# Kernel optimization log

Measured on AMD Instinct MI355X. Metric: run time of the kernel, lower is better.

The kernel has to match this reference:

```python
import jax, jax.numpy as jnp
import numpy as np

N = 4096          # n_assets
D_MODEL = 512
DK = 128
EMB_DIM = 32
QC = 4.0          # quantization_coeff
NUM_EMB = int(np.floor((N - 1) / QC)) + 1  # 1024


def setup_inputs() -> dict:
    key = jax.random.key(0)
    ks = jax.random.split(key, 9)

    def lin_w(k, out_d, in_d):
        # torch nn.Linear default init ~ U(-1/sqrt(in_d), 1/sqrt(in_d))
        b = 1.0 / np.sqrt(in_d)
        return jax.random.uniform(k, (out_d, in_d), jnp.float32, -b, b)

    return {
        "stock_reprs": jax.random.normal(ks[0], (N, D_MODEL), jnp.float32),
        "price_rising_ranks": jax.random.uniform(ks[1], (N,), jnp.float32, 0.0, float(N)),
        "Wq_w": lin_w(ks[2], DK, D_MODEL), "Wq_b": jnp.zeros((DK,), jnp.float32),
        "Wk_w": lin_w(ks[3], DK, D_MODEL), "Wk_b": jnp.zeros((DK,), jnp.float32),
        "Wv_w": lin_w(ks[4], D_MODEL, D_MODEL), "Wv_b": jnp.zeros((D_MODEL,), jnp.float32),
        "rank_emb": jax.random.normal(ks[5], (NUM_EMB, EMB_DIM), jnp.float32),
        "wL_w": lin_w(ks[6], 1, EMB_DIM), "wL_b": jnp.zeros((1,), jnp.float32),
        "wf_w": lin_w(ks[7], 1, D_MODEL), "wf_b": jnp.zeros((1,), jnp.float32),
    }


def reference(stock_reprs, price_rising_ranks, Wq_w, Wq_b, Wk_w, Wk_b,
              Wv_w, Wv_b, rank_emb, wL_w, wL_b, wf_w, wf_b):
    # QKV projections: [N, dk], [N, dk], [N, d_model]
    q = stock_reprs @ Wq_w.T + Wq_b
    k = stock_reprs @ Wk_w.T + Wk_b
    v = stock_reprs @ Wv_w.T + Wv_b

    # Quantized pairwise rank-distance indices [N, N]
    diff = jnp.abs(price_rising_ranks[:, None] - price_rising_ranks[None, :])
    d_ij = jnp.clip(jnp.floor(diff / QC).astype(jnp.int32), 0, NUM_EMB - 1)

    # Gate per quantized distance: sigmoid(w_L(Emb[d])). Precompute the
    # [NUM_EMB] table instead of materializing the [N, N, EMB_DIM] gather
    # (same math: the lookup-then-linear commutes with the gather).
    gate_table = jax.nn.sigmoid(rank_emb @ wL_w[0] + wL_b[0])  # [NUM_EMB]
    psi = gate_table[d_ij]                                     # [N, N]

    score = (q @ k.T) / np.sqrt(float(DK))                     # [N, N]
    att = jax.nn.softmax(psi * score, axis=-1)                 # [N, N]
    a = att @ v                                                # [N, d_model]
    return jax.nn.sigmoid(a @ wf_w[0] + wf_b[0])               # [N]
```

## Files before the change

kernel.cpp:

```cpp
#include <hip/hip_runtime.h>

#define N_ASSETS 4096
#define DMODEL 512
#define DKQ 128
#define NUM_EMB 1024

typedef float f32x4 __attribute__((ext_vector_type(4)));
typedef short s16x8 __attribute__((ext_vector_type(8)));

__device__ __forceinline__ unsigned short f2bf(float x) {
    unsigned u = __float_as_uint(x);
    u += 0x7FFF + ((u >> 16) & 1);
    return (unsigned short)(u >> 16);
}

__device__ __forceinline__ s16x8 ld8(const unsigned short* p) {
    return *(const s16x8*)p;
}

__global__ __launch_bounds__(256) void k_prep(const float* __restrict__ remb,
                                              const float* __restrict__ wLw,
                                              const float* __restrict__ wLb,
                                              const float* __restrict__ Wq,
                                              const float* __restrict__ Wk,
                                              const float* __restrict__ bq,
                                              const float* __restrict__ bk,
                                              const float* __restrict__ Wv,
                                              const float* __restrict__ bv,
                                              const float* __restrict__ wfw,
                                              float* __restrict__ gate,
                                              unsigned short* __restrict__ Wb,
                                              float* __restrict__ bias,
                                              float* __restrict__ weff) {
    int bid = blockIdx.x;
    int tid = threadIdx.x;
    if (bid < 4) {
        int e = bid * 256 + tid;
        float s = wLb[0];
#pragma unroll
        for (int j = 0; j < 32; ++j) s += remb[e * 32 + j] * wLw[j];
        gate[e] = 1.f / (1.f + __expf(-s));
    } else if (bid < 132) {
        int gid = (bid - 4) * 256 + tid;
        int i4 = gid * 4;
        int row = i4 >> 9;
        int col = i4 & 511;
        const float* src; int r;
        if (row < 128) { src = Wq; r = row; } else { src = Wk; r = row - 128; }
        float4 v = *(const float4*)(src + r * 512 + col);
        ushort4 o;
        o.x = f2bf(v.x); o.y = f2bf(v.y); o.z = f2bf(v.z); o.w = f2bf(v.w);
        *(ushort4*)(Wb + i4) = o;
        if (gid < 256) bias[gid] = (gid < 128) ? bq[gid] : bk[gid - 128];
    } else if (bid < 134) {
        __shared__ float wf_s[512];
        wf_s[tid] = wfw[tid];
        wf_s[tid + 256] = wfw[tid + 256];
        __syncthreads();
        int din = (bid - 132) * 256 + tid;
        float a0 = 0.f, a1 = 0.f, a2 = 0.f, a3 = 0.f;
        for (int dout = 0; dout < 512; dout += 4) {
            a0 += Wv[(dout + 0) * 512 + din] * wf_s[dout + 0];
            a1 += Wv[(dout + 1) * 512 + din] * wf_s[dout + 1];
            a2 += Wv[(dout + 2) * 512 + din] * wf_s[dout + 2];
            a3 += Wv[(dout + 3) * 512 + din] * wf_s[dout + 3];
        }
        weff[din] = (a0 + a1) + (a2 + a3);
    } else {
        if (tid < 64) {
            float s = 0.f;
#pragma unroll
            for (int j = 0; j < 8; ++j) s += bv[tid * 8 + j] * wfw[tid * 8 + j];
#pragma unroll
            for (int m = 1; m < 64; m <<= 1) s += __shfl_xor(s, m);
            if (tid == 0) weff[512] = s;
        }
    }
}

__global__ void k_convx(const float* __restrict__ X, unsigned short* __restrict__ Xb, int n) {
    int i4 = (blockIdx.x * 256 + threadIdx.x) * 4;
    if (i4 < n) {
        float4 v = *(const float4*)(X + i4);
        ushort4 o;
        o.x = f2bf(v.x); o.y = f2bf(v.y); o.z = f2bf(v.z); o.w = f2bf(v.w);
        *(ushort4*)(Xb + i4) = o;
    }
}

__global__ __launch_bounds__(256) void k_qk(const unsigned short* __restrict__ Xb,
                                            const unsigned short* __restrict__ Wb,
                                            const float* __restrict__ bias,
                                            unsigned short* __restrict__ qb,
                                            unsigned short* __restrict__ kb) {
    int tid = threadIdx.x;
    int lane = tid & 63, w = tid >> 6;
    int l15 = lane & 15, lhi = lane >> 4;
    int m0 = blockIdx.x * 64 + w * 16;
    int n0 = blockIdx.y * 64;

    f32x4 zero4 = {0.f, 0.f, 0.f, 0.f};
    f32x4 acc[4];
#pragma unroll
    for (int s = 0; s < 4; ++s) acc[s] = zero4;

    const unsigned short* arow = Xb + (m0 + l15) * 512 + lhi * 8;
    for (int k0 = 0; k0 < 512; k0 += 32) {
        s16x8 af = ld8(arow + k0);
#pragma unroll
        for (int s = 0; s < 4; ++s) {
            s16x8 bf = ld8(Wb + (n0 + 16 * s + l15) * 512 + k0 + lhi * 8);
            acc[s] = __builtin_amdgcn_mfma_f32_16x16x32_bf16(af, bf, acc[s], 0, 0, 0);
        }
    }
#pragma unroll
    for (int s = 0; s < 4; ++s) {
        int n = n0 + 16 * s + l15;
        float bv_ = bias[n];
#pragma unroll
        for (int r = 0; r < 4; ++r) {
            int m = m0 + lhi * 4 + r;
            unsigned short val = f2bf(acc[s][r] + bv_);
            if (n < 128) qb[m * 128 + n] = val;
            else         kb[m * 128 + (n - 128)] = val;
        }
    }
}

__global__ __launch_bounds__(256) void k_ugemv(const float* __restrict__ X,
                                               const float* __restrict__ weff,
                                               float* __restrict__ u) {
    int lane = threadIdx.x & 63, w = threadIdx.x >> 6;
    int row = blockIdx.x * 4 + w;
    const float4* ap = (const float4*)(X + row * 512 + lane * 8);
    const float4* wp = (const float4*)(weff + lane * 8);
    float4 a0 = ap[0], a1 = ap[1], w0 = wp[0], w1 = wp[1];
    float s = a0.x * w0.x + a0.y * w0.y + a0.z * w0.z + a0.w * w0.w
            + a1.x * w1.x + a1.y * w1.y + a1.z * w1.z + a1.w * w1.w;
#pragma unroll
    for (int m = 1; m < 64; m <<= 1) s += __shfl_xor(s, m);
    if (lane == 0) u[row] = s + weff[512];
}

__global__ __launch_bounds__(256) void k_score(const unsigned short* __restrict__ qb,
                                               const unsigned short* __restrict__ kb,
                                               const float* __restrict__ ranks,
                                               const float* __restrict__ gate,
                                               const float* __restrict__ u,
                                               float* __restrict__ num_part,
                                               float* __restrict__ den_part) {
    __shared__ float g_lds[NUM_EMB];
    __shared__ float rr[128], rc[128], uc[128];
    int tid = threadIdx.x;
    int lane = tid & 63, w = tid >> 6;
    int l15 = lane & 15, lhi = lane >> 4;
    int wm = w >> 1, wn = w & 1;
    int bm = blockIdx.x, bn = blockIdx.y;

    for (int i = tid; i < NUM_EMB; i += 256) g_lds[i] = gate[i];
    if (tid < 128) {
        rr[tid] = ranks[bm * 128 + tid];
        rc[tid] = ranks[bn * 128 + tid];
        uc[tid] = u[bn * 128 + tid];
    }
    __syncthreads();

    int row0 = wm * 64;
    int col0 = wn * 64;

    f32x4 zero4 = {0.f, 0.f, 0.f, 0.f};
    f32x4 acc[4][4];
#pragma unroll
    for (int mi = 0; mi < 4; ++mi)
#pragma unroll
        for (int ni = 0; ni < 4; ++ni) acc[mi][ni] = zero4;

#pragma unroll
    for (int k0 = 0; k0 < DKQ; k0 += 32) {
        s16x8 af[4], bf[4];
#pragma unroll
        for (int mi = 0; mi < 4; ++mi)
            af[mi] = ld8(qb + (bm * 128 + row0 + mi * 16 + l15) * DKQ + k0 + lhi * 8);
#pragma unroll
        for (int ni = 0; ni < 4; ++ni)
            bf[ni] = ld8(kb + (bn * 128 + col0 + ni * 16 + l15) * DKQ + k0 + lhi * 8);
#pragma unroll
        for (int mi = 0; mi < 4; ++mi)
#pragma unroll
            for (int ni = 0; ni < 4; ++ni)
                acc[mi][ni] = __builtin_amdgcn_mfma_f32_16x16x32_bf16(af[mi], bf[ni], acc[mi][ni], 0, 0, 0);
    }

    const float scale = 0.08838834764831845f;
    float num[4][4], den[4][4];
#pragma unroll
    for (int mi = 0; mi < 4; ++mi)
#pragma unroll
        for (int r = 0; r < 4; ++r) { num[mi][r] = 0.f; den[mi][r] = 0.f; }

#pragma unroll
    for (int mi = 0; mi < 4; ++mi) {
#pragma unroll
        for (int ni = 0; ni < 4; ++ni) {
            int coll = col0 + ni * 16 + l15;
            float rj = rc[coll];
            float uj = uc[coll];
#pragma unroll
            for (int r = 0; r < 4; ++r) {
                int rowl = row0 + mi * 16 + lhi * 4 + r;
                float s = acc[mi][ni][r] * scale;
                float diff = fabsf(rr[rowl] - rj);
                int d = min((int)(diff * 0.25f), NUM_EMB - 1);
                float p = __expf(g_lds[d] * s);
                den[mi][r] += p;
                num[mi][r] += p * uj;
            }
        }
    }
#pragma unroll
    for (int mi = 0; mi < 4; ++mi) {
#pragma unroll
        for (int r = 0; r < 4; ++r) {
            float vn = num[mi][r], vd = den[mi][r];
            vn += __shfl_xor(vn, 1); vd += __shfl_xor(vd, 1);
            vn += __shfl_xor(vn, 2); vd += __shfl_xor(vd, 2);
            vn += __shfl_xor(vn, 4); vd += __shfl_xor(vd, 4);
            vn += __shfl_xor(vn, 8); vd += __shfl_xor(vd, 8);
            if (l15 == 0) {
                int row = bm * 128 + row0 + mi * 16 + lhi * 4 + r;
                num_part[(bn * 2 + wn) * N_ASSETS + row] = vn;
                den_part[(bn * 2 + wn) * N_ASSETS + row] = vd;
            }
        }
    }
}

__global__ __launch_bounds__(256) void k_out(const float* __restrict__ num_part,
                                             const float* __restrict__ den_part,
                                             const float* __restrict__ wfb,
                                             float* __restrict__ out) {
    int lane = threadIdx.x & 63, w = threadIdx.x >> 6;
    int row = blockIdx.x * 4 + w;
    float vn = num_part[lane * N_ASSETS + row];
    float vd = den_part[lane * N_ASSETS + row];
#pragma unroll
    for (int m = 1; m < 64; m <<= 1) {
        vn += __shfl_xor(vn, m);
        vd += __shfl_xor(vd, m);
    }
    if (lane == 0) out[row] = 1.f / (1.f + __expf(-(vn / vd + wfb[0])));
}

extern "C" void kernel_launch(void* const* d_in, const int* in_sizes, int n_in,
                              void* d_out, int out_size, void* d_ws, size_t ws_size,
                              hipStream_t stream) {
    const float* X    = (const float*)d_in[0];
    const float* rks  = (const float*)d_in[1];
    const float* Wq_w = (const float*)d_in[2];
    const float* Wq_b = (const float*)d_in[3];
    const float* Wk_w = (const float*)d_in[4];
    const float* Wk_b = (const float*)d_in[5];
    const float* Wv_w = (const float*)d_in[6];
    const float* Wv_b = (const float*)d_in[7];
    const float* remb = (const float*)d_in[8];
    const float* wL_w = (const float*)d_in[9];
    const float* wL_b = (const float*)d_in[10];
    const float* wf_w = (const float*)d_in[11];
    const float* wf_b = (const float*)d_in[12];
    float* out = (float*)d_out;
    char* ws = (char*)d_ws;

    const size_t OFF_GATE = 0;
    const size_t OFF_BIAS = 4096;
    const size_t OFF_WEFF = 8192;
    const size_t OFF_XB   = 12288;
    const size_t OFF_WB   = OFF_XB + 4194304;
    const size_t OFF_QB   = OFF_WB + 262144;
    const size_t OFF_KB   = OFF_QB + 1048576;
    const size_t OFF_U    = OFF_KB + 1048576;
    const size_t OFF_NUM  = OFF_U + 16384;
    const size_t OFF_DEN  = OFF_NUM + 1048576;

    float* gate = (float*)(ws + OFF_GATE);
    float* bias = (float*)(ws + OFF_BIAS);
    float* weff = (float*)(ws + OFF_WEFF);
    unsigned short* Xb = (unsigned short*)(ws + OFF_XB);
    unsigned short* Wb = (unsigned short*)(ws + OFF_WB);
    unsigned short* qb = (unsigned short*)(ws + OFF_QB);
    unsigned short* kb = (unsigned short*)(ws + OFF_KB);
    float* u = (float*)(ws + OFF_U);
    float* num_part = (float*)(ws + OFF_NUM);
    float* den_part = (float*)(ws + OFF_DEN);

    k_prep<<<135, 256, 0, stream>>>(remb, wL_w, wL_b, Wq_w, Wk_w, Wq_b, Wk_b,
                                    Wv_w, Wv_b, wf_w, gate, Wb, bias, weff);
    k_convx<<<2048, 256, 0, stream>>>(X, Xb, N_ASSETS * DMODEL);
    k_qk<<<dim3(64, 4), 256, 0, stream>>>(Xb, Wb, bias, qb, kb);
    k_ugemv<<<1024, 256, 0, stream>>>(X, weff, u);
    k_score<<<dim3(32, 32), 256, 0, stream>>>(qb, kb, rks, gate, u, num_part, den_part);
    k_out<<<1024, 256, 0, stream>>>(num_part, den_part, wf_b, out);
}
```

Before: 71.71 us.

## Fuse X conversion, QK projection and u GEMV into one projection kernel

```diff
diff --git a/kernel.cpp b/kernel.cpp
--- a/kernel.cpp
+++ b/kernel.cpp
@@ -1,10 +1,13 @@
 #include <hip/hip_runtime.h>
+#include <hip/hip_bf16.h>
 
 #define N_ASSETS 4096
 #define DMODEL 512
 #define DKQ 128
 #define NUM_EMB 1024
 
+#define SCLQ 0.12752789f
+
 typedef float f32x4 __attribute__((ext_vector_type(4)));
 typedef short s16x8 __attribute__((ext_vector_type(8)));
 
@@ -12,6 +15,11 @@
     unsigned u = __float_as_uint(x);
     u += 0x7FFF + ((u >> 16) & 1);
     return (unsigned short)(u >> 16);
+}
+
+__device__ __forceinline__ unsigned pk2(float lo, float hi) {
+    __hip_bfloat162 h = __float22bfloat162_rn(make_float2(lo, hi));
+    return *(unsigned*)&h;
 }
 
 __device__ __forceinline__ s16x8 ld8(const unsigned short* p) {
@@ -52,20 +60,29 @@
         o.x = f2bf(v.x); o.y = f2bf(v.y); o.z = f2bf(v.z); o.w = f2bf(v.w);
         *(ushort4*)(Wb + i4) = o;
         if (gid < 256) bias[gid] = (gid < 128) ? bq[gid] : bk[gid - 128];
-    } else if (bid < 134) {
+    } else if (bid < 148) {
         __shared__ float wf_s[512];
+        __shared__ float part[8][32];
         wf_s[tid] = wfw[tid];
         wf_s[tid + 256] = wfw[tid + 256];
         __syncthreads();
-        int din = (bid - 132) * 256 + tid;
-        float a0 = 0.f, a1 = 0.f, a2 = 0.f, a3 = 0.f;
-        for (int dout = 0; dout < 512; dout += 4) {
-            a0 += Wv[(dout + 0) * 512 + din] * wf_s[dout + 0];
-            a1 += Wv[(dout + 1) * 512 + din] * wf_s[dout + 1];
-            a2 += Wv[(dout + 2) * 512 + din] * wf_s[dout + 2];
-            a3 += Wv[(dout + 3) * 512 + din] * wf_s[dout + 3];
-        }
-        weff[din] = (a0 + a1) + (a2 + a3);
+        int din = (bid - 132) * 32 + (tid & 31);
+        int slice = tid >> 5;
+        const float* wp = Wv + din;
+        float a = 0.f;
+#pragma unroll 4
+        for (int j = 0; j < 64; ++j) {
+            int dout = slice * 64 + j;
+            a += wp[(size_t)dout * 512] * wf_s[dout];
+        }
+        part[slice][tid & 31] = a;
+        __syncthreads();
+        if (tid < 32) {
+            float s = 0.f;
+#pragma unroll
+            for (int sl = 0; sl < 8; ++sl) s += part[sl][tid];
+            weff[(bid - 132) * 32 + tid] = s;
+        }
     } else {
         if (tid < 64) {
             float s = 0.f;
@@ -78,68 +95,74 @@
     }
 }
 
-__global__ void k_convx(const float* __restrict__ X, unsigned short* __restrict__ Xb, int n) {
-    int i4 = (blockIdx.x * 256 + threadIdx.x) * 4;
-    if (i4 < n) {
-        float4 v = *(const float4*)(X + i4);
-        ushort4 o;
-        o.x = f2bf(v.x); o.y = f2bf(v.y); o.z = f2bf(v.z); o.w = f2bf(v.w);
-        *(ushort4*)(Xb + i4) = o;
-    }
-}
-
-__global__ __launch_bounds__(256) void k_qk(const unsigned short* __restrict__ Xb,
-                                            const unsigned short* __restrict__ Wb,
-                                            const float* __restrict__ bias,
-                                            unsigned short* __restrict__ qb,
-                                            unsigned short* __restrict__ kb) {
+__global__ __launch_bounds__(256) void k_proj(const float* __restrict__ X,
+                                              const float* __restrict__ weff,
+                                              const unsigned short* __restrict__ Wb,
+                                              const float* __restrict__ bias,
+                                              unsigned short* __restrict__ qb,
+                                              unsigned short* __restrict__ kb,
+                                              float* __restrict__ u) {
     int tid = threadIdx.x;
     int lane = tid & 63, w = tid >> 6;
     int l15 = lane & 15, lhi = lane >> 4;
-    int m0 = blockIdx.x * 64 + w * 16;
-    int n0 = blockIdx.y * 64;
-
+    int m0 = blockIdx.x * 16;
+
+    const float* xrow = X + (size_t)(m0 + l15) * DMODEL + lhi * 8;
+    const float* wrow = weff + lhi * 8;
+
+    s16x8 af[16];
+    float us = 0.f;
+    bool dou = (w == 0);
+#pragma unroll
+    for (int kc = 0; kc < 16; ++kc) {
+        float4 a = *(const float4*)(xrow + kc * 32);
+        float4 b = *(const float4*)(xrow + kc * 32 + 4);
+        if (dou) {
+            float4 wa = *(const float4*)(wrow + kc * 32);
+            float4 wb = *(const float4*)(wrow + kc * 32 + 4);
+            us += a.x * wa.x + a.y * wa.y + a.z * wa.z + a.w * wa.w
+                + b.x * wb.x + b.y * wb.y + b.z * wb.z + b.w * wb.w;
+        }
+        union { s16x8 v; unsigned q[4]; } fr;
+        fr.q[0] = pk2(a.x, a.y);
+        fr.q[1] = pk2(a.z, a.w);
+        fr.q[2] = pk2(b.x, b.y);
+        fr.q[3] = pk2(b.z, b.w);
+        af[kc] = fr.v;
+    }
+    if (dou) {
+        us += __shfl_xor(us, 16);
+        us += __shfl_xor(us, 32);
+        if (lane < 16) u[m0 + lane] = us + weff[512];
+    }
+
+    int n0w = w * 64;
     f32x4 zero4 = {0.f, 0.f, 0.f, 0.f};
     f32x4 acc[4];
 #pragma unroll
-    for (int s = 0; s < 4; ++s) acc[s] = zero4;
-
-    const unsigned short* arow = Xb + (m0 + l15) * 512 + lhi * 8;
-    for (int k0 = 0; k0 < 512; k0 += 32) {
-        s16x8 af = ld8(arow + k0);
-#pragma unroll
-        for (int s = 0; s < 4; ++s) {
-            s16x8 bf = ld8(Wb + (n0 + 16 * s + l15) * 512 + k0 + lhi * 8);
-            acc[s] = __builtin_amdgcn_mfma_f32_16x16x32_bf16(af, bf, acc[s], 0, 0, 0);
-        }
-    }
-#pragma unroll
-    for (int s = 0; s < 4; ++s) {
-        int n = n0 + 16 * s + l15;
+    for (int ni = 0; ni < 4; ++ni) acc[ni] = zero4;
+
+#pragma unroll
+    for (int k0 = 0; k0 < 16; ++k0) {
+#pragma unroll
+        for (int ni = 0; ni < 4; ++ni) {
+            s16x8 bf = ld8(Wb + (size_t)(n0w + ni * 16 + l15) * 512 + k0 * 32 + lhi * 8);
+            acc[ni] = __builtin_amdgcn_mfma_f32_16x16x32_bf16(af[k0], bf, acc[ni], 0, 0, 0);
+        }
+    }
+
+#pragma unroll
+    for (int ni = 0; ni < 4; ++ni) {
+        int n = n0w + ni * 16 + l15;
         float bv_ = bias[n];
 #pragma unroll
         for (int r = 0; r < 4; ++r) {
             int m = m0 + lhi * 4 + r;
-            unsigned short val = f2bf(acc[s][r] + bv_);
-            if (n < 128) qb[m * 128 + n] = val;
-            else         kb[m * 128 + (n - 128)] = val;
-        }
-    }
-}
-
-__global__ __launch_bounds__(256) void k_ugemv(const float* __restrict__ X,
-                                               const float* __restrict__ weff,
-                                               float* __restrict__ u) {
-    int lane = threadIdx.x & 63, w = threadIdx.x >> 6;
-    int row = blockIdx.x * 4 + w;
-    const float4* ap = (const float4*)(X + row * 512 + lane * 8);
-    const float4* wp = (const float4*)(weff + lane * 8);
-    float4 a0 = ap[0], a1 = ap[1], w0 = wp[0], w1 = wp[1];
-    float s = a0.x * w0.x + a0.y * w0.y + a0.z * w0.z + a0.w * w0.w
-            + a1.x * w1.x + a1.y * w1.y + a1.z * w1.z + a1.w * w1.w;
-#pragma unroll
-    for (int m = 1; m < 64; m <<= 1) s += __shfl_xor(s, m);
-    if (lane == 0) u[row] = s + weff[512];
+            float v = acc[ni][r] + bv_;
+            if (n < 128) qb[m * 128 + n] = f2bf(v * SCLQ);
+            else         kb[m * 128 + (n - 128)] = f2bf(v);
+        }
+    }
 }
 
 __global__ __launch_bounds__(256) void k_score(const unsigned short* __restrict__ qb,
@@ -191,7 +214,6 @@
                 acc[mi][ni] = __builtin_amdgcn_mfma_f32_16x16x32_bf16(af[mi], bf[ni], acc[mi][ni], 0, 0, 0);
     }
 
-    const float scale = 0.08838834764831845f;
     float num[4][4], den[4][4];
 #pragma unroll
     for (int mi = 0; mi < 4; ++mi)
@@ -208,10 +230,9 @@
 #pragma unroll
             for (int r = 0; r < 4; ++r) {
                 int rowl = row0 + mi * 16 + lhi * 4 + r;
-                float s = acc[mi][ni][r] * scale;
                 float diff = fabsf(rr[rowl] - rj);
                 int d = min((int)(diff * 0.25f), NUM_EMB - 1);
-                float p = __expf(g_lds[d] * s);
+                float p = exp2f(g_lds[d] * acc[mi][ni][r]);
                 den[mi][r] += p;
                 num[mi][r] += p * uj;
             }
@@ -273,8 +294,7 @@
     const size_t OFF_GATE = 0;
     const size_t OFF_BIAS = 4096;
     const size_t OFF_WEFF = 8192;
-    const size_t OFF_XB   = 12288;
-    const size_t OFF_WB   = OFF_XB + 4194304;
+    const size_t OFF_WB   = 12288;
     const size_t OFF_QB   = OFF_WB + 262144;
     const size_t OFF_KB   = OFF_QB + 1048576;
     const size_t OFF_U    = OFF_KB + 1048576;
@@ -284,7 +304,6 @@
     float* gate = (float*)(ws + OFF_GATE);
     float* bias = (float*)(ws + OFF_BIAS);
     float* weff = (float*)(ws + OFF_WEFF);
-    unsigned short* Xb = (unsigned short*)(ws + OFF_XB);
     unsigned short* Wb = (unsigned short*)(ws + OFF_WB);
     unsigned short* qb = (unsigned short*)(ws + OFF_QB);
     unsigned short* kb = (unsigned short*)(ws + OFF_KB);
@@ -292,11 +311,9 @@
     float* num_part = (float*)(ws + OFF_NUM);
     float* den_part = (float*)(ws + OFF_DEN);
 
-    k_prep<<<135, 256, 0, stream>>>(remb, wL_w, wL_b, Wq_w, Wk_w, Wq_b, Wk_b,
+    k_prep<<<149, 256, 0, stream>>>(remb, wL_w, wL_b, Wq_w, Wk_w, Wq_b, Wk_b,
                                     Wv_w, Wv_b, wf_w, gate, Wb, bias, weff);
-    k_convx<<<2048, 256, 0, stream>>>(X, Xb, N_ASSETS * DMODEL);
-    k_qk<<<dim3(64, 4), 256, 0, stream>>>(Xb, Wb, bias, qb, kb);
-    k_ugemv<<<1024, 256, 0, stream>>>(X, weff, u);
+    k_proj<<<256, 256, 0, stream>>>(X, weff, Wb, bias, qb, kb, u);
     k_score<<<dim3(32, 32), 256, 0, stream>>>(qb, kb, rks, gate, u, num_part, den_part);
     k_out<<<1024, 256, 0, stream>>>(num_part, den_part, wf_b, out);
 }
```

Result: no change. 71.73 us (+0.0%).
